# Performance work log

Hardware: AMD Instinct MI355X
Metric: run time of the kernel (lower is better)

Reference implementation:

```python
import jax, jax.numpy as jnp
import numpy as np

FH = FW = 3          # field_height, field_width
SF = 2               # scale_factor passed to set_transforms
NODES = 32           # out_channels
D_IN = 16            # in_channels (field depth)
HID = 32             # mlpnodes[0]; mlpnodes = [32, 1]


def maxpool_3x3_s2_p1(x):
    # Deterministic stand-in for FractionalMaxPool2d(kernel=3, output=(H//2, W//2)):
    return jax.lax.reduce_window(
        x, -jnp.inf, jax.lax.max,
        window_dimensions=(1, 1, 3, 3),
        window_strides=(1, 1, 2, 2),
        padding=((0, 0), (0, 0), (1, 1), (1, 1)))


def unfold_3x3(x):
    # torch.nn.Unfold(kernel=(3,3), padding=1): (N,D,H,W) -> (N, D, 9, H*W)
    N, D, H, W = x.shape
    xp = jnp.pad(x, ((0, 0), (0, 0), (1, 1), (1, 1)))
    patches = jnp.stack([xp[:, :, i:i + H, j:j + W]
                         for i in range(3) for j in range(3)], axis=2)
    return patches.reshape(N, D, 9, H * W)


def setup_inputs() -> dict:
    key = jax.random.key(0)
    k = jax.random.split(key, 6)
    N, H, W = 32, 96, 96
    x = jax.random.normal(k[0], (N, D_IN, H, W), dtype=jnp.float32)
    # S per node: xavier_uniform on shape (1, D, 3, 3): fan_in=D*9, fan_out=1*9
    bound_S = float(np.sqrt(6.0 / (D_IN * 9 + 9)))
    S = jax.random.uniform(k[1], (NODES, D_IN, FH, FW), jnp.float32, -bound_S, bound_S)
    # per-node MLP: Linear(D_IN -> HID) -> ReLU -> Linear(HID -> 1) -> ReLU
    b1w = 1.0 / np.sqrt(D_IN)
    W1 = jax.random.uniform(k[2], (NODES, D_IN, HID), jnp.float32, -b1w, b1w)
    b1 = jax.random.uniform(k[3], (NODES, HID), jnp.float32, -b1w, b1w)
    b2w = 1.0 / np.sqrt(HID)
    W2 = jax.random.uniform(k[4], (NODES, HID, 1), jnp.float32, -b2w, b2w)
    b2 = jax.random.uniform(k[5], (NODES, 1), jnp.float32, -b2w, b2w)
    return {"x": x, "S": S, "W1": W1, "b1": b1, "W2": W2, "b2": b2}


def reference(x, S, W1, b1, W2, b2):
    N, D, H, W = x.shape
    Hs, Ws = H // SF, W // SF
    U = unfold_3x3(maxpool_3x3_s2_p1(x))            # (N, D, 9, L), L = Hs*Ws
    Sf = S.reshape(S.shape[0], D, FH * FW)          # (O, D, 9)
    # StructFun: M[n,d,l] = sum_k S[d,k] * U[n,d,k,l], batched over nodes o
    M = jnp.einsum('odk,ndkl->nlod', Sf, U)         # (N, L, O, D)
    # StructBlock: reshape to (N,Hs,Ws,D) then per-node MLP over last dim
    h = jax.nn.relu(jnp.einsum('nlod,odh->nloh', M, W1) + b1)   # (N, L, O, HID)
    y = jax.nn.relu(jnp.einsum('nloh,ohe->nloe', h, W2) + b2)   # (N, L, O, 1)
    out = y[..., 0].reshape(N, Hs, Ws, -1)          # (N, Hs, Ws, O)
    return out.transpose(0, 3, 1, 2)                # (N, O, Hs, Ws)
```

## Files before the change

### kernel.cpp

```cpp
#include <hip/hip_runtime.h>
#include <math.h>

typedef __bf16 bf16;
typedef __bf16 bf16x8 __attribute__((ext_vector_type(8)));
typedef float  f32x16 __attribute__((ext_vector_type(16)));

#define D_INC 16
#define NODES 32
#define HID   32
#define HS    48
#define WSZ   48
#define NPX   (HS*WSZ)
#define H_IN  96
#define W_IN  96
#define N_B   32

#define MP_BLOCKS   1152
#define WPRE_BLOCKS 640

__global__ __launch_bounds__(256) void pre_kernel(
    const float* __restrict__ x, bf16* __restrict__ Pg,
    const float* __restrict__ S, const float* __restrict__ W1,
    const float* __restrict__ b1, bf16* __restrict__ Wp)
{
    if (blockIdx.x < MP_BLOCKS) {
        int idx = blockIdx.x * 256 + threadIdx.x;
        int c  = idx % WSZ;
        int t  = idx / WSZ;
        int q  = t & 3;
        int rr = t >> 2;
        int r  = rr % HS;
        int n  = rr / HS;

        const float* xb = x + ((size_t)(n * D_INC + q * 4)) * (H_IN * W_IN);

        float m0 = -INFINITY, m1 = -INFINITY, m2 = -INFINITY, m3 = -INFINITY;
        #pragma unroll
        for (int dr = 0; dr < 3; ++dr) {
            int xr = 2 * r - 1 + dr;
            if (xr < 0) continue;
            #pragma unroll
            for (int dc = 0; dc < 3; ++dc) {
                int xc = 2 * c - 1 + dc;
                if (xc < 0) continue;
                const float* p = xb + xr * W_IN + xc;
                m0 = fmaxf(m0, p[0 * H_IN * W_IN]);
                m1 = fmaxf(m1, p[1 * H_IN * W_IN]);
                m2 = fmaxf(m2, p[2 * H_IN * W_IN]);
                m3 = fmaxf(m3, p[3 * H_IN * W_IN]);
            }
        }
        union { bf16 h[4]; uint2 u; } v;
        v.h[0] = (bf16)m0; v.h[1] = (bf16)m1; v.h[2] = (bf16)m2; v.h[3] = (bf16)m3;
        *(uint2*)(Pg + ((size_t)((n * HS + r) * WSZ + c)) * D_INC + q * 4) = v.u;
    } else {
        int idx = (blockIdx.x - MP_BLOCKS) * 256 + threadIdx.x;
        if (idx >= NODES * 10 * 2 * HID * 8) return;
        int j  = idx & 7;
        int h  = (idx >> 3) & 31;
        int qp = (idx >> 8) & 1;
        int os = idx >> 9;
        int s  = os % 10;
        int o  = os / 10;
        int k  = 16 * s + 8 * qp + j;
        float v = 0.f;
        if (k < 144) {
            int t = k >> 4;
            int d = k & 15;
            v = S[(o * D_INC + d) * 9 + t] * W1[(o * D_INC + d) * HID + h];
        } else if (k == 144) {
            v = b1[o * HID + h];
        }
        Wp[idx] = (bf16)v;
    }
}

__global__ __launch_bounds__(256, 2) void gemm_kernel(
    const bf16* __restrict__ Pg, const bf16* __restrict__ Wp,
    const float* __restrict__ W2, const float* __restrict__ b2,
    float* __restrict__ out)
{
    __shared__ __align__(16) bf16  Pl[8 * 50 * D_INC];
    __shared__ __align__(16) bf16  Wl[4 * 10 * 512];
    __shared__ __align__(16) float W2l[4 * HID];

    const int b    = blockIdx.x;
    const int n    = blockIdx.y;
    const int ob   = blockIdx.z * 4;
    const int tid  = threadIdx.x;
    const int lane = tid & 63;
    const int w    = tid >> 6;
    const int ln31 = lane & 31;
    const int qp   = lane >> 5;

    const int px0     = b * 256;
    const int r_start = px0 / 48;

    const uint4 z4 = make_uint4(0u, 0u, 0u, 0u);

    {
        const uint4* src = (const uint4*)(Wp + (size_t)ob * 10 * 512);
        uint4*       dst = (uint4*)Wl;
        #pragma unroll
        for (int i = 0; i < 10; ++i)
            dst[i * 256 + tid] = src[i * 256 + tid];
    }

    for (int u = tid; u < 768; u += 256) {
        int half = u & 1;
        int colu = (u >> 1) % 48;
        int row  = (u >> 1) / 48;
        int pr   = r_start - 1 + row;
        uint4 v  = z4;
        if (pr >= 0 && pr < HS)
            v = *(const uint4*)(Pg + ((size_t)(n * HS + pr) * WSZ + colu) * D_INC + half * 8);
        *(uint4*)(Pl + (row * 50 + colu + 1) * D_INC + half * 8) = v;
    }
    if (tid < 32) {
        int row  = tid >> 2;
        int side = (tid >> 1) & 1;
        int half = tid & 1;
        *(uint4*)(Pl + (row * 50 + side * 49) * D_INC + half * 8) = z4;
        ((float4*)W2l)[tid] = ((const float4*)(W2 + ob * HID))[tid];
    }
    __syncthreads();

    int base_ad[2];
    int pxg[2];
    #pragma unroll
    for (int t = 0; t < 2; ++t) {
        int px = px0 + w * 64 + t * 32 + ln31;
        int r  = px / 48;
        int c  = px - r * 48;
        int rl = r - r_start;
        base_ad[t] = ((rl * 50) + c) * 32 + qp * 16;
        pxg[t] = px;
    }

    bf16x8 Bf[2][10];
    #pragma unroll
    for (int t = 0; t < 2; ++t) {
        #pragma unroll
        for (int s = 0; s < 9; ++s) {
            const int di = s / 3, dj = s % 3;
            Bf[t][s] = *(const bf16x8*)((const char*)Pl + base_ad[t] + (di * 50 + dj) * 32);
        }
        bf16x8 bias = {};
        if (qp == 0) bias[0] = (bf16)1.0f;
        Bf[t][9] = bias;
    }

    for (int o4 = 0; o4 < 4; ++o4) {
        const int o = ob + o4;

        bf16x8 Af[10];
        #pragma unroll
        for (int s = 0; s < 10; ++s)
            Af[s] = *(const bf16x8*)(Wl + (o4 * 10 + s) * 512 + lane * 8);

        f32x16 acc0 = {};
        f32x16 acc1 = {};
        #pragma unroll
        for (int s = 0; s < 10; ++s) {
            acc0 = __builtin_amdgcn_mfma_f32_32x32x16_bf16(Af[s], Bf[0][s], acc0, 0, 0, 0);
            acc1 = __builtin_amdgcn_mfma_f32_32x32x16_bf16(Af[s], Bf[1][s], acc1, 0, 0, 0);
        }

        const float* w2b = W2l + o4 * HID + 4 * qp;
        float4 w2v0 = *(const float4*)(w2b);
        float4 w2v1 = *(const float4*)(w2b + 8);
        float4 w2v2 = *(const float4*)(w2b + 16);
        float4 w2v3 = *(const float4*)(w2b + 24);
        const float bb = b2[o];

        #pragma unroll
        for (int t = 0; t < 2; ++t) {
            const f32x16 a = t ? acc1 : acc0;
            float part;
            part  = fmaxf(a[0],  0.f) * w2v0.x;
            part  = fmaf(fmaxf(a[1],  0.f), w2v0.y, part);
            part  = fmaf(fmaxf(a[2],  0.f), w2v0.z, part);
            part  = fmaf(fmaxf(a[3],  0.f), w2v0.w, part);
            part  = fmaf(fmaxf(a[4],  0.f), w2v1.x, part);
            part  = fmaf(fmaxf(a[5],  0.f), w2v1.y, part);
            part  = fmaf(fmaxf(a[6],  0.f), w2v1.z, part);
            part  = fmaf(fmaxf(a[7],  0.f), w2v1.w, part);
            part  = fmaf(fmaxf(a[8],  0.f), w2v2.x, part);
            part  = fmaf(fmaxf(a[9],  0.f), w2v2.y, part);
            part  = fmaf(fmaxf(a[10], 0.f), w2v2.z, part);
            part  = fmaf(fmaxf(a[11], 0.f), w2v2.w, part);
            part  = fmaf(fmaxf(a[12], 0.f), w2v3.x, part);
            part  = fmaf(fmaxf(a[13], 0.f), w2v3.y, part);
            part  = fmaf(fmaxf(a[14], 0.f), w2v3.z, part);
            part  = fmaf(fmaxf(a[15], 0.f), w2v3.w, part);
            float tot = part + __shfl_xor(part, 32);
            tot = fmaxf(tot + bb, 0.f);
            if (qp == 0)
                out[(size_t)(n * NODES + o) * NPX + pxg[t]] = tot;
        }
    }
}

extern "C" void kernel_launch(void* const* d_in, const int* in_sizes, int n_in,
                              void* d_out, int out_size, void* d_ws, size_t ws_size,
                              hipStream_t stream)
{
    const float* x  = (const float*)d_in[0];
    const float* S  = (const float*)d_in[1];
    const float* W1 = (const float*)d_in[2];
    const float* b1 = (const float*)d_in[3];
    const float* W2 = (const float*)d_in[4];
    const float* b2 = (const float*)d_in[5];
    float* out = (float*)d_out;

    bf16* Pg = (bf16*)d_ws;
    bf16* Wp = (bf16*)((char*)d_ws + (size_t)N_B * NPX * D_INC * 2);

    pre_kernel<<<MP_BLOCKS + WPRE_BLOCKS, 256, 0, stream>>>(x, Pg, S, W1, b1, Wp);

    dim3 grid(9, N_B, 8);
    gemm_kernel<<<grid, 256, 0, stream>>>(Pg, Wp, W2, b2, out);
}
```

Measured before the change: 104.5 us.

## Retile GEMM blocks to half-image rows with register-held weights for two nodes

The GEMM kernel now gives each block 24 output rows (1152 pixels) and 2 nodes instead of 256 pixels and 4 nodes. Weight fragments and W2/b2 are loaded straight from global memory into registers, not staged through shared memory. The pooled tile is stored split by channel half to change the LDS layout. Each wave loops over 9 pixel tiles that reuse the register-held weights. The aim is to cut redundant halo and weight staging per block and amortise setup over more MFMA work, at the cost of fewer blocks (1024 vs 2304) and more register pressure.

```diff
diff --git a/kernel.cpp b/kernel.cpp
--- a/kernel.cpp
+++ b/kernel.cpp
@@ -50,8 +50,8 @@
                 m3 = fmaxf(m3, p[3 * H_IN * W_IN]);
             }
         }
-        union { bf16 h[4]; uint2 u; } v;
-        v.h[0] = (bf16)m0; v.h[1] = (bf16)m1; v.h[2] = (bf16)m2; v.h[3] = (bf16)m3;
+        union { bf16 hh[4]; uint2 u; } v;
+        v.hh[0] = (bf16)m0; v.hh[1] = (bf16)m1; v.hh[2] = (bf16)m2; v.hh[3] = (bf16)m3;
         *(uint2*)(Pg + ((size_t)((n * HS + r) * WSZ + c)) * D_INC + q * 4) = v.u;
     } else {
         int idx = (blockIdx.x - MP_BLOCKS) * 256 + threadIdx.x;
@@ -80,123 +80,113 @@
     const float* __restrict__ W2, const float* __restrict__ b2,
     float* __restrict__ out)
 {
-    __shared__ __align__(16) bf16  Pl[8 * 50 * D_INC];
-    __shared__ __align__(16) bf16  Wl[4 * 10 * 512];
-    __shared__ __align__(16) float W2l[4 * HID];
-
-    const int b    = blockIdx.x;
+    __shared__ __align__(16) bf16 Pl[26 * 2 * 50 * 8];
+
+    const int hb   = blockIdx.x;
     const int n    = blockIdx.y;
-    const int ob   = blockIdx.z * 4;
+    const int ob   = blockIdx.z * 2;
     const int tid  = threadIdx.x;
     const int lane = tid & 63;
     const int w    = tid >> 6;
     const int ln31 = lane & 31;
     const int qp   = lane >> 5;
 
-    const int px0     = b * 256;
-    const int r_start = px0 / 48;
+    const int r0 = hb * 24;
 
     const uint4 z4 = make_uint4(0u, 0u, 0u, 0u);
 
-    {
-        const uint4* src = (const uint4*)(Wp + (size_t)ob * 10 * 512);
-        uint4*       dst = (uint4*)Wl;
-        #pragma unroll
-        for (int i = 0; i < 10; ++i)
-            dst[i * 256 + tid] = src[i * 256 + tid];
-    }
-
-    for (int u = tid; u < 768; u += 256) {
+    for (int u = tid; u < 26 * 48 * 2; u += 256) {
         int half = u & 1;
-        int colu = (u >> 1) % 48;
+        int c    = (u >> 1) % 48;
         int row  = (u >> 1) / 48;
-        int pr   = r_start - 1 + row;
+        int pr   = r0 - 1 + row;
         uint4 v  = z4;
         if (pr >= 0 && pr < HS)
-            v = *(const uint4*)(Pg + ((size_t)(n * HS + pr) * WSZ + colu) * D_INC + half * 8);
-        *(uint4*)(Pl + (row * 50 + colu + 1) * D_INC + half * 8) = v;
-    }
-    if (tid < 32) {
+            v = *(const uint4*)(Pg + ((size_t)(n * HS + pr) * WSZ + c) * D_INC + half * 8);
+        *(uint4*)(Pl + ((row * 2 + half) * 50 + (c + 1)) * 8) = v;
+    }
+    if (tid < 104) {
         int row  = tid >> 2;
-        int side = (tid >> 1) & 1;
-        int half = tid & 1;
-        *(uint4*)(Pl + (row * 50 + side * 49) * D_INC + half * 8) = z4;
-        ((float4*)W2l)[tid] = ((const float4*)(W2 + ob * HID))[tid];
+        int half = (tid >> 1) & 1;
+        int side = tid & 1;
+        *(uint4*)(Pl + ((row * 2 + half) * 50 + side * 49) * 8) = z4;
     }
     __syncthreads();
 
-    int base_ad[2];
-    int pxg[2];
+    bf16x8 Af[2][10];
     #pragma unroll
-    for (int t = 0; t < 2; ++t) {
-        int px = px0 + w * 64 + t * 32 + ln31;
-        int r  = px / 48;
-        int c  = px - r * 48;
-        int rl = r - r_start;
-        base_ad[t] = ((rl * 50) + c) * 32 + qp * 16;
-        pxg[t] = px;
-    }
-
-    bf16x8 Bf[2][10];
+    for (int e = 0; e < 2; ++e) {
+        const bf16* wp = Wp + (size_t)((ob + e) * 10) * 512 + lane * 8;
+        #pragma unroll
+        for (int s = 0; s < 10; ++s)
+            Af[e][s] = *(const bf16x8*)(wp + s * 512);
+    }
+    float4 w2v[2][4];
+    float  bb[2];
     #pragma unroll
-    for (int t = 0; t < 2; ++t) {
+    for (int e = 0; e < 2; ++e) {
+        const float* w2b = W2 + (ob + e) * HID + 4 * qp;
+        w2v[e][0] = *(const float4*)(w2b);
+        w2v[e][1] = *(const float4*)(w2b + 8);
+        w2v[e][2] = *(const float4*)(w2b + 16);
+        w2v[e][3] = *(const float4*)(w2b + 24);
+        bb[e] = b2[ob + e];
+    }
+
+    const int    p_base   = w * 288 + ln31;
+    const size_t outbase0 = (size_t)(n * NODES + ob) * NPX + hb * 1152;
+
+    #pragma unroll
+    for (int ti = 0; ti < 9; ++ti) {
+        const int p  = p_base + ti * 32;
+        const int rl = p / 48;
+        const int c  = p - rl * 48;
+        const int base_ch = (rl * 2 + qp) * 50 + c;
+
+        bf16x8 Bf[10];
         #pragma unroll
         for (int s = 0; s < 9; ++s) {
             const int di = s / 3, dj = s % 3;
-            Bf[t][s] = *(const bf16x8*)((const char*)Pl + base_ad[t] + (di * 50 + dj) * 32);
-        }
-        bf16x8 bias = {};
-        if (qp == 0) bias[0] = (bf16)1.0f;
-        Bf[t][9] = bias;
-    }
-
-    for (int o4 = 0; o4 < 4; ++o4) {
-        const int o = ob + o4;
-
-        bf16x8 Af[10];
-        #pragma unroll
-        for (int s = 0; s < 10; ++s)
-            Af[s] = *(const bf16x8*)(Wl + (o4 * 10 + s) * 512 + lane * 8);
+            Bf[s] = *(const bf16x8*)(Pl + (base_ch + di * 100 + dj) * 8);
+        }
+        {
+            bf16x8 bias = {};
+            if (qp == 0) bias[0] = (bf16)1.0f;
+            Bf[9] = bias;
+        }
 
         f32x16 acc0 = {};
         f32x16 acc1 = {};
         #pragma unroll
         for (int s = 0; s < 10; ++s) {
-            acc0 = __builtin_amdgcn_mfma_f32_32x32x16_bf16(Af[s], Bf[0][s], acc0, 0, 0, 0);
-            acc1 = __builtin_amdgcn_mfma_f32_32x32x16_bf16(Af[s], Bf[1][s], acc1, 0, 0, 0);
-        }
-
-        const float* w2b = W2l + o4 * HID + 4 * qp;
-        float4 w2v0 = *(const float4*)(w2b);
-        float4 w2v1 = *(const float4*)(w2b + 8);
-        float4 w2v2 = *(const float4*)(w2b + 16);
-        float4 w2v3 = *(const float4*)(w2b + 24);
-        const float bb = b2[o];
-
-        #pragma unroll
-        for (int t = 0; t < 2; ++t) {
-            const f32x16 a = t ? acc1 : acc0;
+            acc0 = __builtin_amdgcn_mfma_f32_32x32x16_bf16(Af[0][s], Bf[s], acc0, 0, 0, 0);
+            acc1 = __builtin_amdgcn_mfma_f32_32x32x16_bf16(Af[1][s], Bf[s], acc1, 0, 0, 0);
+        }
+
+        #pragma unroll
+        for (int e = 0; e < 2; ++e) {
+            const f32x16 a = e ? acc1 : acc0;
             float part;
-            part  = fmaxf(a[0],  0.f) * w2v0.x;
-            part  = fmaf(fmaxf(a[1],  0.f), w2v0.y, part);
-            part  = fmaf(fmaxf(a[2],  0.f), w2v0.z, part);
-            part  = fmaf(fmaxf(a[3],  0.f), w2v0.w, part);
-            part  = fmaf(fmaxf(a[4],  0.f), w2v1.x, part);
-            part  = fmaf(fmaxf(a[5],  0.f), w2v1.y, part);
-            part  = fmaf(fmaxf(a[6],  0.f), w2v1.z, part);
-            part  = fmaf(fmaxf(a[7],  0.f), w2v1.w, part);
-            part  = fmaf(fmaxf(a[8],  0.f), w2v2.x, part);
-            part  = fmaf(fmaxf(a[9],  0.f), w2v2.y, part);
-            part  = fmaf(fmaxf(a[10], 0.f), w2v2.z, part);
-            part  = fmaf(fmaxf(a[11], 0.f), w2v2.w, part);
-            part  = fmaf(fmaxf(a[12], 0.f), w2v3.x, part);
-            part  = fmaf(fmaxf(a[13], 0.f), w2v3.y, part);
-            part  = fmaf(fmaxf(a[14], 0.f), w2v3.z, part);
-            part  = fmaf(fmaxf(a[15], 0.f), w2v3.w, part);
+            part  = fmaxf(a[0],  0.f) * w2v[e][0].x;
+            part  = fmaf(fmaxf(a[1],  0.f), w2v[e][0].y, part);
+            part  = fmaf(fmaxf(a[2],  0.f), w2v[e][0].z, part);
+            part  = fmaf(fmaxf(a[3],  0.f), w2v[e][0].w, part);
+            part  = fmaf(fmaxf(a[4],  0.f), w2v[e][1].x, part);
+            part  = fmaf(fmaxf(a[5],  0.f), w2v[e][1].y, part);
+            part  = fmaf(fmaxf(a[6],  0.f), w2v[e][1].z, part);
+            part  = fmaf(fmaxf(a[7],  0.f), w2v[e][1].w, part);
+            part  = fmaf(fmaxf(a[8],  0.f), w2v[e][2].x, part);
+            part  = fmaf(fmaxf(a[9],  0.f), w2v[e][2].y, part);
+            part  = fmaf(fmaxf(a[10], 0.f), w2v[e][2].z, part);
+            part  = fmaf(fmaxf(a[11], 0.f), w2v[e][2].w, part);
+            part  = fmaf(fmaxf(a[12], 0.f), w2v[e][3].x, part);
+            part  = fmaf(fmaxf(a[13], 0.f), w2v[e][3].y, part);
+            part  = fmaf(fmaxf(a[14], 0.f), w2v[e][3].z, part);
+            part  = fmaf(fmaxf(a[15], 0.f), w2v[e][3].w, part);
             float tot = part + __shfl_xor(part, 32);
-            tot = fmaxf(tot + bb, 0.f);
+            tot = fmaxf(tot + bb[e], 0.f);
             if (qp == 0)
-                out[(size_t)(n * NODES + o) * NPX + pxg[t]] = tot;
+                out[outbase0 + (size_t)e * NPX + p] = tot;
         }
     }
 }
@@ -218,6 +208,6 @@
 
     pre_kernel<<<MP_BLOCKS + WPRE_BLOCKS, 256, 0, stream>>>(x, Pg, S, W1, b1, Wp);
 
-    dim3 grid(9, N_B, 8);
+    dim3 grid(2, N_B, 16);
     gemm_kernel<<<grid, 256, 0, stream>>>(Pg, Wp, W2, b2, out);
 }
```

Result: no change. 104.6 us (+0.1%).
